# Kernel optimization log

Hardware: AMD Instinct MI355X
Metric: run time of the kernel (lower is better)

Reference implementation:

```python
import jax, jax.numpy as jnp
import numpy as np

NUM_HEADS = 8
NUM_GROUPS = 32
EPS = 1e-5


def setup_inputs() -> dict:
    key = jax.random.key(0)
    ks = jax.random.split(key, 6)
    C = 512
    scale = 1.0 / np.sqrt(C)
    return {
        "q": jax.random.normal(ks[0], (2, C, 64, 64), dtype=jnp.float32),
        "gn_w": jnp.ones((C,), jnp.float32),
        "gn_b": jnp.zeros((C,), jnp.float32),
        "wq": jax.random.normal(ks[1], (C, C), jnp.float32) * scale,
        "bq": jnp.zeros((C,), jnp.float32),
        "wk": jax.random.normal(ks[2], (C, C), jnp.float32) * scale,
        "bk": jnp.zeros((C,), jnp.float32),
        "wv": jax.random.normal(ks[3], (C, C), jnp.float32) * scale,
        "bv": jnp.zeros((C,), jnp.float32),
        "wo": jax.random.normal(ks[4], (C, C), jnp.float32) * scale,
        "bo": jnp.zeros((C,), jnp.float32),
    }


def _group_norm(x, w, b):
    # x: [B, C, H, W]
    B, C, H, W = x.shape
    xg = x.reshape(B, NUM_GROUPS, C // NUM_GROUPS, H, W)
    mean = xg.mean(axis=(2, 3, 4), keepdims=True)
    var = xg.var(axis=(2, 3, 4), keepdims=True)
    xn = ((xg - mean) * jax.lax.rsqrt(var + EPS)).reshape(B, C, H, W)
    return xn * w[None, :, None, None] + b[None, :, None, None]


def reference(q, gn_w, gn_b, wq, bq, wk, bk, wv, bv, wo, bo):
    B, C, H, W = q.shape
    hd = C // NUM_HEADS
    resid = q
    x = _group_norm(q, gn_w, gn_b)
    x = x.reshape(B, C, H * W).transpose(0, 2, 1)  # [B, N, C]
    # torch Linear: y = x @ W.T + b  (self-attention: k = v = x)
    qp = x @ wq.T + bq
    kp = x @ wk.T + bk
    vp = x @ wv.T + bv
    N = H * W
    def split(t):  # [B, N, C] -> [B, h, N, hd]
        return t.reshape(B, N, NUM_HEADS, hd).transpose(0, 2, 1, 3)
    qh, kh, vh = split(qp), split(kp), split(vp)
    scores = jnp.einsum('bhnc,bhmc->bhnm', qh, kh) / jnp.sqrt(jnp.float32(hd))
    attn = jax.nn.softmax(scores, axis=-1)
    out = jnp.einsum('bhnm,bhmc->bhnc', attn, vh)
    out = out.transpose(0, 2, 1, 3).reshape(B, N, C)
    out = out @ wo.T + bo
    out2d = out.transpose(0, 2, 1).reshape(B, C, H, W)
    return out2d + resid
```

## Files before the change

### kernel.cpp

```cpp
#include <hip/hip_runtime.h>
#include <hip/hip_bf16.h>
#include <cstdint>
#include <cstddef>

using bf16x8   = __attribute__((ext_vector_type(8))) short;
using f32x4    = __attribute__((ext_vector_type(4))) float;
using f32x16   = __attribute__((ext_vector_type(16))) float;
using ushort8  = __attribute__((ext_vector_type(8))) unsigned short;
using ushort4v = __attribute__((ext_vector_type(4))) unsigned short;
using float4v  = __attribute__((ext_vector_type(4))) float;
using float2v  = __attribute__((ext_vector_type(2))) float;

#define MFMA16(a,b,c) __builtin_amdgcn_mfma_f32_16x16x32_bf16((a),(b),(c),0,0,0)
#define MFMA32(a,b,c) __builtin_amdgcn_mfma_f32_32x32x16_bf16((a),(b),(c),0,0,0)

#define QSCALE 0.18033688011112042f

__device__ __forceinline__ unsigned short f2bf(float f){
    union { float f; unsigned u; } v; v.f = f;
    unsigned r = v.u + 0x7FFFu + ((v.u >> 16) & 1u);
    return (unsigned short)(r >> 16);
}

__device__ __forceinline__ int cvtpk(float lo, float hi){
    int r;
    asm volatile("v_cvt_pk_bf16_f32 %0, %1, %2" : "=v"(r) : "v"(lo), "v"(hi));
    return r;
}

#if __has_builtin(__builtin_amdgcn_permlane32_swap)
__device__ __forceinline__ void plswap(int &a, int &b){
    auto r = __builtin_amdgcn_permlane32_swap(a, b, false, false);
    a = r[0]; b = r[1];
}
#else
__device__ __forceinline__ void plswap(int &a, int &b){
    int ta = __shfl_xor(a, 32), tb = __shfl_xor(b, 32);
    bool hi = ((threadIdx.x & 63) >= 32);
    int na = hi ? tb : a;
    int nb = hi ? b  : ta;
    a = na; b = nb;
}
#endif

__device__ __forceinline__ void gload16(const unsigned short* g, unsigned short* l){
    __builtin_amdgcn_global_load_lds(
        (const __attribute__((address_space(1))) void*)g,
        (__attribute__((address_space(3))) void*)l,
        16, 0, 0);
}

__global__ __launch_bounds__(256) void gn_stats_wconv(const float* __restrict__ x,
                                                      float2v* __restrict__ parts,
                                                      const float* __restrict__ w0, const float* __restrict__ w1,
                                                      const float* __restrict__ w2, const float* __restrict__ w3,
                                                      unsigned short* wqk, unsigned short* wv, unsigned short* wo){
    int bid = blockIdx.x;
    if (bid < 512){
        const float4v* p4 = (const float4v*)(x + (size_t)bid * 8192);
        float s = 0.f, ss = 0.f;
        #pragma unroll
        for (int i = 0; i < 8; i++){
            float4v v = p4[i*256 + threadIdx.x];
            s  += v[0]+v[1]+v[2]+v[3];
            ss += v[0]*v[0]+v[1]*v[1]+v[2]*v[2]+v[3]*v[3];
        }
        __shared__ float ls[4], lss[4];
        int lane = threadIdx.x & 63, w = threadIdx.x >> 6;
        #pragma unroll
        for (int o = 32; o > 0; o >>= 1){ s += __shfl_down(s, o); ss += __shfl_down(ss, o); }
        if (lane == 0){ ls[w] = s; lss[w] = ss; }
        __syncthreads();
        if (threadIdx.x == 0){
            float2v p;
            p[0] = ls[0]+ls[1]+ls[2]+ls[3];
            p[1] = lss[0]+lss[1]+lss[2]+lss[3];
            parts[bid] = p;
        }
    } else {
        int i2 = bid - 512;
        int y = i2 >> 8, bx = i2 & 255;
        const float* src; unsigned short* dst; float sc = 1.0f;
        switch (y){
            case 0: src = w0; dst = wqk;          sc = QSCALE; break;
            case 1: src = w1; dst = wqk + 512*512; break;
            case 2: src = w2; dst = wv; break;
            default: src = w3; dst = wo; break;
        }
        int i = (bx*256 + threadIdx.x) * 4;
        float4v v = *(const float4v*)(src + i);
        ushort4v o;
        #pragma unroll
        for (int j = 0; j < 4; j++) o[j] = f2bf(v[j]*sc);
        *(ushort4v*)(dst + i) = o;
    }
}

__global__ __launch_bounds__(256) void gn_apply(const float* __restrict__ x,
                                                const float2v* __restrict__ parts,
                                                const float* __restrict__ gw,
                                                const float* __restrict__ gb,
                                                unsigned short* __restrict__ xn){
    int b = blockIdx.z, c0 = blockIdx.y * 64, n0 = blockIdx.x * 64;
    __shared__ unsigned short tile[64][68];
    __shared__ float gmean[4], grstd[4];
    if (threadIdx.x < 4){
        int g = b*32 + (c0 >> 4) + threadIdx.x;
        float s = 0.f, ss = 0.f;
        #pragma unroll
        for (int e = 0; e < 8; e++){
            float2v p = parts[g*8 + e];
            s += p[0]; ss += p[1];
        }
        float m = s * (1.f/65536.f);
        float var = ss * (1.f/65536.f) - m*m;
        gmean[threadIdx.x] = m;
        grstd[threadIdx.x] = rsqrtf(var + 1e-5f);
    }
    __syncthreads();
    for (int i = threadIdx.x; i < 64*16; i += 256){
        int row = i >> 4, f4 = i & 15;
        int c = c0 + row;
        int gl = row >> 4;
        float rs = grstd[gl];
        float wgt = gw[c] * rs;
        float bia = gb[c] - gmean[gl] * wgt;
        float4v v = *(const float4v*)(x + ((size_t)(b*512 + c))*4096 + n0 + f4*4);
        ushort4v o;
        #pragma unroll
        for (int j = 0; j < 4; j++) o[j] = f2bf(v[j]*wgt + bia);
        *(ushort4v*)&tile[row][f4*4] = o;
    }
    __syncthreads();
    for (int i = threadIdx.x; i < 64*8; i += 256){
        int nr = i >> 3, c8 = i & 7;
        ushort8 o;
        #pragma unroll
        for (int j = 0; j < 8; j++) o[j] = tile[c8*8 + j][nr];
        *(ushort8*)(xn + ((size_t)(b*4096 + n0 + nr))*512 + c0 + c8*8) = o;
    }
}

__global__ __launch_bounds__(256) void gemm_qkv(const unsigned short* __restrict__ xn,
                                                const unsigned short* __restrict__ wqk,
                                                const unsigned short* __restrict__ Wv,
                                                const float* __restrict__ bq,
                                                const float* __restrict__ bk,
                                                const float* __restrict__ bv,
                                                unsigned short* __restrict__ Q,
                                                unsigned short* __restrict__ K,
                                                unsigned short* __restrict__ Vt){
    __shared__ unsigned short Al[128*32];
    __shared__ unsigned short Bl[128*32];
    int bid = blockIdx.x;
    int t = threadIdx.x, lane = t & 63, w = t >> 6;
    int wr = w >> 1, wc = w & 1;
    int lr = lane >> 2, lc = lane & 3;

    if (bid < 512){
        int m0 = (bid & 63) * 128, n0 = (bid >> 6) * 128;
        f32x4 acc[4][4] = {};
        const unsigned short* Asrc = xn  + (size_t)(m0 + w*32 + lr)*512 + lc*8;
        const unsigned short* Bsrc = wqk + (size_t)(n0 + w*32 + lr)*512 + lc*8;
        unsigned short* Adst = &Al[(w*32)*32];
        unsigned short* Bdst = &Bl[(w*32)*32];

        for (int ks = 0; ks < 16; ks++){
            gload16(Asrc + ks*32,          Adst);
            gload16(Asrc + ks*32 + 16*512, Adst + 16*32);
            gload16(Bsrc + ks*32,          Bdst);
            gload16(Bsrc + ks*32 + 16*512, Bdst + 16*32);
            asm volatile("s_waitcnt vmcnt(0)" ::: "memory");
            __syncthreads();
            bf16x8 a[4], b[4];
            #pragma unroll
            for (int mi = 0; mi < 4; mi++) a[mi] = *(bf16x8*)&Al[(wr*64 + mi*16 + (lane&15))*32 + (lane>>4)*8];
            #pragma unroll
            for (int ni = 0; ni < 4; ni++) b[ni] = *(bf16x8*)&Bl[(wc*64 + ni*16 + (lane&15))*32 + (lane>>4)*8];
            #pragma unroll
            for (int mi = 0; mi < 4; mi++)
                #pragma unroll
                for (int ni = 0; ni < 4; ni++)
                    acc[mi][ni] = MFMA16(a[mi], b[ni], acc[mi][ni]);
            __syncthreads();
        }

        int cK = n0 >> 9;
        const float* bias = cK ? bk : bq;
        unsigned short* dst0 = cK ? K : Q;
        float bsc = cK ? 1.0f : QSCALE;
        #pragma unroll
        for (int mi = 0; mi < 4; mi++)
            #pragma unroll
            for (int ni = 0; ni < 4; ni++)
                #pragma unroll
                for (int r = 0; r < 4; r++){
                    int mrow = m0 + wr*64 + mi*16 + (lane>>4)*4 + r;
                    int col  = (n0 & 511) + wc*64 + ni*16 + (lane&15);
                    int b_ = mrow >> 12, n = mrow & 4095;
                    int h = col >> 6, d = col & 63;
                    float v = acc[mi][ni][r] + bias[col]*bsc;
                    dst0[(size_t)((b_*8+h)*4096 + n)*64 + d] = f2bf(v);
                }
    } else {
        int i2 = bid - 512;
        int m0 = (i2 >> 6) * 64, n0 = (i2 & 63) * 128;
        f32x4 acc[2][4] = {};
        const unsigned short* Asrc = Wv + (size_t)(m0 + w*16 + lr)*512 + lc*8;
        const unsigned short* Bsrc = xn + (size_t)(n0 + w*32 + lr)*512 + lc*8;
        unsigned short* Adst = &Al[(w*16)*32];
        unsigned short* Bdst = &Bl[(w*32)*32];

        for (int ks = 0; ks < 16; ks++){
            gload16(Asrc + ks*32,          Adst);
            gload16(Bsrc + ks*32,          Bdst);
            gload16(Bsrc + ks*32 + 16*512, Bdst + 16*32);
            asm volatile("s_waitcnt vmcnt(0)" ::: "memory");
            __syncthreads();
            bf16x8 a[2], b[4];
            #pragma unroll
            for (int mi = 0; mi < 2; mi++) a[mi] = *(bf16x8*)&Al[(wr*32 + mi*16 + (lane&15))*32 + (lane>>4)*8];
            #pragma unroll
            for (int ni = 0; ni < 4; ni++) b[ni] = *(bf16x8*)&Bl[(wc*64 + ni*16 + (lane&15))*32 + (lane>>4)*8];
            #pragma unroll
            for (int mi = 0; mi < 2; mi++)
                #pragma unroll
                for (int ni = 0; ni < 4; ni++)
                    acc[mi][ni] = MFMA16(a[mi], b[ni], acc[mi][ni]);
            __syncthreads();
        }
        #pragma unroll
        for (int mi = 0; mi < 2; mi++)
            #pragma unroll
            for (int ni = 0; ni < 4; ni++)
                #pragma unroll
                for (int r = 0; r < 4; r++){
                    int row  = m0 + wr*32 + mi*16 + (lane>>4)*4 + r;
                    int colm = n0 + wc*64 + ni*16 + (lane&15);
                    int b_ = colm >> 12, n = colm & 4095;
                    int h = row >> 6, d = row & 63;
                    float v = acc[mi][ni][r] + bv[row];
                    Vt[(size_t)((b_*8+h)*64 + d)*4096 + n] = f2bf(v);
                }
    }
}

__global__ __launch_bounds__(256) void gemm_o2(const unsigned short* __restrict__ Wo,
                                               const unsigned short* __restrict__ Om,
                                               const float* __restrict__ bo,
                                               const float* __restrict__ resid,
                                               float* __restrict__ outp){
    __shared__ unsigned short Al[64*32];
    __shared__ unsigned short Bl[128*32];
    int t = threadIdx.x, lane = t & 63, w = t >> 6;
    int wr = w >> 1, wc = w & 1;
    int m0 = blockIdx.y * 64, n0 = blockIdx.x * 128;
    int lr = lane >> 2, lc = lane & 3;
    f32x4 acc[2][4] = {};

    const unsigned short* Asrc = Wo + (size_t)(m0 + w*16 + lr)*512 + lc*8;
    const unsigned short* Bsrc = Om + (size_t)(n0 + w*32 + lr)*512 + lc*8;
    unsigned short* Adst = &Al[(w*16)*32];
    unsigned short* Bdst = &Bl[(w*32)*32];

    for (int ks = 0; ks < 16; ks++){
        gload16(Asrc + ks*32,          Adst);
        gload16(Bsrc + ks*32,          Bdst);
        gload16(Bsrc + ks*32 + 16*512, Bdst + 16*32);
        asm volatile("s_waitcnt vmcnt(0)" ::: "memory");
        __syncthreads();
        bf16x8 a[2], b[4];
        #pragma unroll
        for (int mi = 0; mi < 2; mi++) a[mi] = *(bf16x8*)&Al[(wr*32 + mi*16 + (lane&15))*32 + (lane>>4)*8];
        #pragma unroll
        for (int ni = 0; ni < 4; ni++) b[ni] = *(bf16x8*)&Bl[(wc*64 + ni*16 + (lane&15))*32 + (lane>>4)*8];
        #pragma unroll
        for (int mi = 0; mi < 2; mi++)
            #pragma unroll
            for (int ni = 0; ni < 4; ni++)
                acc[mi][ni] = MFMA16(a[mi], b[ni], acc[mi][ni]);
        __syncthreads();
    }
    #pragma unroll
    for (int mi = 0; mi < 2; mi++)
        #pragma unroll
        for (int ni = 0; ni < 4; ni++)
            #pragma unroll
            for (int r = 0; r < 4; r++){
                int row  = m0 + wr*32 + mi*16 + (lane>>4)*4 + r;
                int colm = n0 + wc*64 + ni*16 + (lane&15);
                int b_ = colm >> 12, n = colm & 4095;
                size_t oi = ((size_t)(b_*512 + row))*4096 + n;
                outp[oi] = acc[mi][ni][r] + bo[row] + resid[oi];
            }
}

__global__ __launch_bounds__(128, 2) void attn9(const unsigned short* __restrict__ Q,
                                                const unsigned short* __restrict__ K,
                                                const unsigned short* __restrict__ Vt,
                                                unsigned short* __restrict__ O){
    int bid = blockIdx.x;
    int idx = bid >> 3;
    int bh = ((bid & 7) << 1) | (idx >> 6);
    int qt = idx & 63;
    int t = threadIdx.x, lane = t & 63, w = t >> 6;
    int ln = lane & 31, hi = lane >> 5;
    int q0 = qt * 64;

    __shared__ unsigned short Kl[2][64*64];
    __shared__ unsigned short Vl[2][2][64*32];

    const unsigned short* Qb = Q  + (size_t)bh * 4096 * 64;
    const unsigned short* Kb = K  + (size_t)bh * 4096 * 64;
    const unsigned short* Vb = Vt + (size_t)bh * 64 * 4096;

    bf16x8 bqa[4], bqb[4];
    #pragma unroll
    for (int dsub = 0; dsub < 4; dsub++){
        bqa[dsub] = *(const bf16x8*)(Qb + (size_t)(q0 + ln)*64      + dsub*16 + hi*8);
        bqb[dsub] = *(const bf16x8*)(Qb + (size_t)(q0 + 32 + ln)*64 + dsub*16 + hi*8);
    }

    int srow = lane >> 3;
    int sswz = (lane & 7) ^ srow;
    int vdl = lane >> 2;
    int vsl = (lane & 3) ^ ((vdl >> 1) & 3);

    auto stage = [&](int kt){
        int kv0 = kt * 64;
        unsigned short* kdst = &Kl[kt & 1][0];
        #pragma unroll
        for (int i = 0; i < 4; i++){
            int r0 = w*32 + i*8;
            gload16(Kb + (size_t)(kv0 + r0 + srow)*64 + sswz*8, kdst + r0*64);
        }
        unsigned short* vdst = &Vl[kt & 1][w][0];
        #pragma unroll
        for (int i = 0; i < 4; i++)
            gload16(Vb + (size_t)(i*16 + vdl)*4096 + kv0 + w*32 + vsl*8, vdst + i*512);
    };

    stage(0);
    stage(1);

    f32x16 o0a, o1a, o0b, o1b, z;
    #pragma unroll
    for (int r = 0; r < 16; r++){ o0a[r]=0.f; o1a[r]=0.f; o0b[r]=0.f; o1b[r]=0.f; z[r]=0.f; }
    float lsA = 0.f, lsB = 0.f;

    const char* KbA = (const char*)&Kl[0][0] + (w*32 + ln)*128;
    int swzr = (ln & 7) << 4;
    const char* VbW = (const char*)&Vl[0][w][0];
    int vrswz = (ln >> 1) & 3;

    for (int kt = 0; kt < 64; kt++){
        if (kt < 63) asm volatile("s_waitcnt vmcnt(8)" ::: "memory");
        else         asm volatile("s_waitcnt vmcnt(0)" ::: "memory");
        __builtin_amdgcn_sched_barrier(0);

        int kboff = (kt & 1) * (64*64*2);
        int vboff = (kt & 1) * (2*64*32*2);

        f32x16 sA, sB;
        {
            int cb = (hi*16) ^ swzr;
            bf16x8 ak = *(const bf16x8*)(KbA + kboff + cb);
            sA = MFMA32(ak, bqa[0], z);
            sB = MFMA32(ak, bqb[0], z);
        }
        __builtin_amdgcn_s_setprio(1);
        #pragma unroll
        for (int dsub = 1; dsub < 4; dsub++){
            int cb = (dsub*32 + hi*16) ^ swzr;
            bf16x8 ak = *(const bf16x8*)(KbA + kboff + cb);
            sA = MFMA32(ak, bqa[dsub], sA);
            sB = MFMA32(ak, bqb[dsub], sB);
        }
        __builtin_amdgcn_s_setprio(0);

        #pragma unroll
        for (int r = 0; r < 16; r++){ sA[r] = __builtin_amdgcn_exp2f(sA[r]); lsA += sA[r]; }
        #pragma unroll
        for (int r = 0; r < 16; r++){ sB[r] = __builtin_amdgcn_exp2f(sB[r]); lsB += sB[r]; }

        __builtin_amdgcn_s_setprio(1);
        #pragma unroll
        for (int hsel = 0; hsel < 2; hsel++){
            int obp = hsel * 8;
            int a0 = cvtpk(sA[obp+0], sA[obp+1]);
            int a1 = cvtpk(sA[obp+2], sA[obp+3]);
            int c0 = cvtpk(sA[obp+4], sA[obp+5]);
            int c1 = cvtpk(sA[obp+6], sA[obp+7]);
            plswap(a0, c0);
            plswap(a1, c1);
            union { int i[4]; bf16x8 v; } fuA;
            fuA.i[0] = a0; fuA.i[1] = a1; fuA.i[2] = c0; fuA.i[3] = c1;

            int d0 = cvtpk(sB[obp+0], sB[obp+1]);
            int d1 = cvtpk(sB[obp+2], sB[obp+3]);
            int e0 = cvtpk(sB[obp+4], sB[obp+5]);
            int e1 = cvtpk(sB[obp+6], sB[obp+7]);
            plswap(d0, e0);
            plswap(d1, e1);
            union { int i[4]; bf16x8 v; } fuB;
            fuB.i[0] = d0; fuB.i[1] = d1; fuB.i[2] = e0; fuB.i[3] = e1;

            int p0 = (((hsel*2 + hi) ^ vrswz) << 4);
            bf16x8 av0 = *(const bf16x8*)(VbW + vboff + ln*64 + p0);
            bf16x8 av1 = *(const bf16x8*)(VbW + vboff + (32 + ln)*64 + p0);
            o0a = MFMA32(av0, fuA.v, o0a);
            o1a = MFMA32(av1, fuA.v, o1a);
            o0b = MFMA32(av0, fuB.v, o0b);
            o1b = MFMA32(av1, fuB.v, o1b);
        }
        __builtin_amdgcn_s_setprio(0);

        __builtin_amdgcn_sched_barrier(0);
        if (kt < 62) stage(kt + 2);
        __builtin_amdgcn_sched_barrier(0);
    }

    lsA += __shfl_xor(lsA, 32);
    lsB += __shfl_xor(lsB, 32);
    __syncthreads();
    float* m1 = (float*)&Kl[0][0];
    float* m2 = (float*)&Vl[0][0][0];
    if (w == 1){
        #pragma unroll
        for (int r = 0; r < 16; r++){
            m1[r*64 + lane]        = o0a[r];
            m1[1024 + r*64 + lane] = o1a[r];
            m2[r*64 + lane]        = o0b[r];
            m2[1024 + r*64 + lane] = o1b[r];
        }
        if (hi == 0){ m2[2048 + ln] = lsA; m2[2048 + 32 + ln] = lsB; }
    }
    __syncthreads();
    if (w == 0){
        #pragma unroll
        for (int r = 0; r < 16; r++){
            o0a[r] += m1[r*64 + lane];
            o1a[r] += m1[1024 + r*64 + lane];
            o0b[r] += m2[r*64 + lane];
            o1b[r] += m2[1024 + r*64 + lane];
        }
        float rA = 1.0f / (lsA + m2[2048 + ln]);
        float rB = 1.0f / (lsB + m2[2048 + 32 + ln]);
        int b = bh >> 3, h = bh & 7;
        unsigned short* dstA = O + (size_t)(b*4096 + q0 + ln)*512      + h*64;
        unsigned short* dstB = O + (size_t)(b*4096 + q0 + 32 + ln)*512 + h*64;
        #pragma unroll
        for (int m = 0; m < 2; m++){
            const f32x16& ovA = m ? o1a : o0a;
            const f32x16& ovB = m ? o1b : o0b;
            #pragma unroll
            for (int g = 0; g < 4; g++){
                int d = m*32 + g*8 + hi*4;
                ushort4v pkA, pkB;
                #pragma unroll
                for (int j = 0; j < 4; j++){
                    pkA[j] = f2bf(ovA[g*4 + j] * rA);
                    pkB[j] = f2bf(ovB[g*4 + j] * rB);
                }
                *(ushort4v*)(dstA + d) = pkA;
                *(ushort4v*)(dstB + d) = pkB;
            }
        }
    }
}

extern "C" void kernel_launch(void* const* d_in, const int* in_sizes, int n_in,
                              void* d_out, int out_size, void* d_ws, size_t ws_size,
                              hipStream_t stream) {
    const float* q    = (const float*)d_in[0];
    const float* gn_w = (const float*)d_in[1];
    const float* gn_b = (const float*)d_in[2];
    const float* wq   = (const float*)d_in[3];
    const float* bq   = (const float*)d_in[4];
    const float* wk   = (const float*)d_in[5];
    const float* bk   = (const float*)d_in[6];
    const float* wv   = (const float*)d_in[7];
    const float* bv   = (const float*)d_in[8];
    const float* wo   = (const float*)d_in[9];
    const float* bo   = (const float*)d_in[10];
    float* outp = (float*)d_out;

    char* ws = (char*)d_ws;
    float2v* parts = (float2v*)ws;
    unsigned short* xn  = (unsigned short*)(ws + 8192);
    const size_t TOK = (size_t)8192 * 512;
    unsigned short* wqkb = xn + TOK;
    unsigned short* wvb  = wqkb + 1024*512;
    unsigned short* wob  = wvb + 512*512;
    unsigned short* Qb   = wob + 512*512;
    unsigned short* Kb   = Qb + TOK;
    unsigned short* Vt   = Kb + TOK;
    unsigned short* Ob   = Vt + TOK;

    gn_stats_wconv<<<1536, 256, 0, stream>>>(q, parts, wq, wk, wv, wo, wqkb, wvb, wob);
    gn_apply<<<dim3(64, 8, 2), 256, 0, stream>>>(q, parts, gn_w, gn_b, xn);
    gemm_qkv<<<1024, 256, 0, stream>>>(xn, wqkb, wvb, bq, bk, bv, Qb, Kb, Vt);
    attn9<<<1024, 128, 0, stream>>>(Qb, Kb, Vt, Ob);
    gemm_o2<<<dim3(64, 8), 256, 0, stream>>>(wob, Ob, bo, q, outp);
}
```

Baseline: 134.2 us.

## Single-buffer V tile in attention to cut LDS and raise occupancy

Turns the V tile from a double buffer into a single buffer. V for step kt+1 is staged right after step kt finishes using V, while K keeps its two-ahead prefetch. This halves the V LDS footprint and raises the launch_bounds minimum blocks per CU from 2 to 3, so more waves can hide latency. In exchange, V loads get only one iteration of lead time, and the wait count is cut to match. The epilogue reduction scratch is remapped to fit the smaller V buffer.

```diff
diff --git a/kernel.cpp b/kernel.cpp
--- a/kernel.cpp
+++ b/kernel.cpp
@@ -295,10 +295,10 @@
             }
 }
 
-__global__ __launch_bounds__(128, 2) void attn9(const unsigned short* __restrict__ Q,
-                                                const unsigned short* __restrict__ K,
-                                                const unsigned short* __restrict__ Vt,
-                                                unsigned short* __restrict__ O){
+__global__ __launch_bounds__(128, 3) void attn10(const unsigned short* __restrict__ Q,
+                                                 const unsigned short* __restrict__ K,
+                                                 const unsigned short* __restrict__ Vt,
+                                                 unsigned short* __restrict__ O){
     int bid = blockIdx.x;
     int idx = bid >> 3;
     int bh = ((bid & 7) << 1) | (idx >> 6);
@@ -308,7 +308,7 @@
     int q0 = qt * 64;
 
     __shared__ unsigned short Kl[2][64*64];
-    __shared__ unsigned short Vl[2][2][64*32];
+    __shared__ unsigned short Vl[2][64*32];
 
     const unsigned short* Qb = Q  + (size_t)bh * 4096 * 64;
     const unsigned short* Kb = K  + (size_t)bh * 4096 * 64;
@@ -326,7 +326,7 @@
     int vdl = lane >> 2;
     int vsl = (lane & 3) ^ ((vdl >> 1) & 3);
 
-    auto stage = [&](int kt){
+    auto stageK = [&](int kt){
         int kv0 = kt * 64;
         unsigned short* kdst = &Kl[kt & 1][0];
         #pragma unroll
@@ -334,14 +334,18 @@
             int r0 = w*32 + i*8;
             gload16(Kb + (size_t)(kv0 + r0 + srow)*64 + sswz*8, kdst + r0*64);
         }
-        unsigned short* vdst = &Vl[kt & 1][w][0];
+    };
+    auto stageV = [&](int kt){
+        int kv0 = kt * 64;
+        unsigned short* vdst = &Vl[w][0];
         #pragma unroll
         for (int i = 0; i < 4; i++)
             gload16(Vb + (size_t)(i*16 + vdl)*4096 + kv0 + w*32 + vsl*8, vdst + i*512);
     };
 
-    stage(0);
-    stage(1);
+    stageK(0);
+    stageV(0);
+    stageK(1);
 
     f32x16 o0a, o1a, o0b, o1b, z;
     #pragma unroll
@@ -350,16 +354,15 @@
 
     const char* KbA = (const char*)&Kl[0][0] + (w*32 + ln)*128;
     int swzr = (ln & 7) << 4;
-    const char* VbW = (const char*)&Vl[0][w][0];
+    const char* VbW = (const char*)&Vl[w][0];
     int vrswz = (ln >> 1) & 3;
 
     for (int kt = 0; kt < 64; kt++){
-        if (kt < 63) asm volatile("s_waitcnt vmcnt(8)" ::: "memory");
+        if (kt < 63) asm volatile("s_waitcnt vmcnt(4)" ::: "memory");
         else         asm volatile("s_waitcnt vmcnt(0)" ::: "memory");
         __builtin_amdgcn_sched_barrier(0);
 
         int kboff = (kt & 1) * (64*64*2);
-        int vboff = (kt & 1) * (2*64*32*2);
 
         f32x16 sA, sB;
         {
@@ -406,8 +409,8 @@
             fuB.i[0] = d0; fuB.i[1] = d1; fuB.i[2] = e0; fuB.i[3] = e1;
 
             int p0 = (((hsel*2 + hi) ^ vrswz) << 4);
-            bf16x8 av0 = *(const bf16x8*)(VbW + vboff + ln*64 + p0);
-            bf16x8 av1 = *(const bf16x8*)(VbW + vboff + (32 + ln)*64 + p0);
+            bf16x8 av0 = *(const bf16x8*)(VbW + ln*64 + p0);
+            bf16x8 av1 = *(const bf16x8*)(VbW + (32 + ln)*64 + p0);
             o0a = MFMA32(av0, fuA.v, o0a);
             o1a = MFMA32(av1, fuA.v, o1a);
             o0b = MFMA32(av0, fuB.v, o0b);
@@ -416,7 +419,8 @@
         __builtin_amdgcn_s_setprio(0);
 
         __builtin_amdgcn_sched_barrier(0);
-        if (kt < 62) stage(kt + 2);
+        if (kt < 63) stageV(kt + 1);
+        if (kt < 62) stageK(kt + 2);
         __builtin_amdgcn_sched_barrier(0);
     }
 
@@ -424,16 +428,16 @@
     lsB += __shfl_xor(lsB, 32);
     __syncthreads();
     float* m1 = (float*)&Kl[0][0];
-    float* m2 = (float*)&Vl[0][0][0];
+    float* m2 = (float*)&Vl[0][0];
     if (w == 1){
         #pragma unroll
         for (int r = 0; r < 16; r++){
             m1[r*64 + lane]        = o0a[r];
             m1[1024 + r*64 + lane] = o1a[r];
-            m2[r*64 + lane]        = o0b[r];
-            m2[1024 + r*64 + lane] = o1b[r];
-        }
-        if (hi == 0){ m2[2048 + ln] = lsA; m2[2048 + 32 + ln] = lsB; }
+            m1[2048 + r*64 + lane] = o0b[r];
+            m1[3072 + r*64 + lane] = o1b[r];
+        }
+        if (hi == 0){ m2[ln] = lsA; m2[32 + ln] = lsB; }
     }
     __syncthreads();
     if (w == 0){
@@ -441,11 +445,11 @@
         for (int r = 0; r < 16; r++){
             o0a[r] += m1[r*64 + lane];
             o1a[r] += m1[1024 + r*64 + lane];
-            o0b[r] += m2[r*64 + lane];
-            o1b[r] += m2[1024 + r*64 + lane];
-        }
-        float rA = 1.0f / (lsA + m2[2048 + ln]);
-        float rB = 1.0f / (lsB + m2[2048 + 32 + ln]);
+            o0b[r] += m1[2048 + r*64 + lane];
+            o1b[r] += m1[3072 + r*64 + lane];
+        }
+        float rA = 1.0f / (lsA + m2[ln]);
+        float rB = 1.0f / (lsB + m2[32 + ln]);
         int b = bh >> 3, h = bh & 7;
         unsigned short* dstA = O + (size_t)(b*4096 + q0 + ln)*512      + h*64;
         unsigned short* dstB = O + (size_t)(b*4096 + q0 + 32 + ln)*512 + h*64;
@@ -500,6 +504,6 @@
     gn_stats_wconv<<<1536, 256, 0, stream>>>(q, parts, wq, wk, wv, wo, wqkb, wvb, wob);
     gn_apply<<<dim3(64, 8, 2), 256, 0, stream>>>(q, parts, gn_w, gn_b, xn);
     gemm_qkv<<<1024, 256, 0, stream>>>(xn, wqkb, wvb, bq, bk, bv, Qb, Kb, Vt);
-    attn9<<<1024, 128, 0, stream>>>(Qb, Kb, Vt, Ob);
+    attn10<<<1024, 128, 0, stream>>>(Qb, Kb, Vt, Ob);
     gemm_o2<<<dim3(64, 8), 256, 0, stream>>>(wob, Ob, bo, q, outp);
 }
```

New measurement: 172.0 us. 28.1% more time.

## Software-pipeline attention loop so next QK^T overlaps current softmax and PV

Applied to the files above, without the earlier changes.

Restructures the attention main loop into a two-tile software pipeline. The QK^T MFMAs for tile t+1 are issued alongside the exp/convert/PV work for tile t, and K and V staging are split so each is fetched on its own schedule. The aim is to keep the matrix units busy while the exp and pack work runs. It adds a second live score accumulator pair, which raises register pressure, and the new waitcnt accounting has to stay correct across the split K/V loads. The setprio hints are dropped.

```diff
diff --git a/kernel.cpp b/kernel.cpp
--- a/kernel.cpp
+++ b/kernel.cpp
@@ -295,10 +295,10 @@
             }
 }
 
-__global__ __launch_bounds__(128, 2) void attn9(const unsigned short* __restrict__ Q,
-                                                const unsigned short* __restrict__ K,
-                                                const unsigned short* __restrict__ Vt,
-                                                unsigned short* __restrict__ O){
+__global__ __launch_bounds__(128, 2) void attn11(const unsigned short* __restrict__ Q,
+                                                 const unsigned short* __restrict__ K,
+                                                 const unsigned short* __restrict__ Vt,
+                                                 unsigned short* __restrict__ O){
     int bid = blockIdx.x;
     int idx = bid >> 3;
     int bh = ((bid & 7) << 1) | (idx >> 6);
@@ -326,7 +326,7 @@
     int vdl = lane >> 2;
     int vsl = (lane & 3) ^ ((vdl >> 1) & 3);
 
-    auto stage = [&](int kt){
+    auto stageK = [&](int kt){
         int kv0 = kt * 64;
         unsigned short* kdst = &Kl[kt & 1][0];
         #pragma unroll
@@ -334,16 +334,16 @@
             int r0 = w*32 + i*8;
             gload16(Kb + (size_t)(kv0 + r0 + srow)*64 + sswz*8, kdst + r0*64);
         }
+    };
+    auto stageV = [&](int kt){
+        int kv0 = kt * 64;
         unsigned short* vdst = &Vl[kt & 1][w][0];
         #pragma unroll
         for (int i = 0; i < 4; i++)
             gload16(Vb + (size_t)(i*16 + vdl)*4096 + kv0 + w*32 + vsl*8, vdst + i*512);
     };
 
-    stage(0);
-    stage(1);
-
-    f32x16 o0a, o1a, o0b, o1b, z;
+    f32x16 o0a, o1a, o0b, o1b, z, sEA, sEB, sOA, sOB;
     #pragma unroll
     for (int r = 0; r < 16; r++){ o0a[r]=0.f; o1a[r]=0.f; o0b[r]=0.f; o1b[r]=0.f; z[r]=0.f; }
     float lsA = 0.f, lsB = 0.f;
@@ -352,73 +352,95 @@
     int swzr = (ln & 7) << 4;
     const char* VbW = (const char*)&Vl[0][w][0];
     int vrswz = (ln >> 1) & 3;
-
-    for (int kt = 0; kt < 64; kt++){
-        if (kt < 63) asm volatile("s_waitcnt vmcnt(8)" ::: "memory");
-        else         asm volatile("s_waitcnt vmcnt(0)" ::: "memory");
+    const int KBUFSZ = 64*64*2;
+    const int VBUFSZ = 2*64*32*2;
+
+#define QKSTEP(SA,SB, KBOFF) { \
+    { int cb = (hi*16) ^ swzr; \
+      bf16x8 ak = *(const bf16x8*)(KbA + (KBOFF) + cb); \
+      SA = MFMA32(ak, bqa[0], z); \
+      SB = MFMA32(ak, bqb[0], z); } \
+    _Pragma("unroll") \
+    for (int dsub = 1; dsub < 4; dsub++){ \
+        int cb = (dsub*32 + hi*16) ^ swzr; \
+        bf16x8 ak = *(const bf16x8*)(KbA + (KBOFF) + cb); \
+        SA = MFMA32(ak, bqa[dsub], SA); \
+        SB = MFMA32(ak, bqb[dsub], SB); \
+    } }
+
+#define FINISH(SA,SB, VBOFF) { \
+    _Pragma("unroll") \
+    for (int r = 0; r < 16; r++){ SA[r] = __builtin_amdgcn_exp2f(SA[r]); lsA += SA[r]; } \
+    _Pragma("unroll") \
+    for (int r = 0; r < 16; r++){ SB[r] = __builtin_amdgcn_exp2f(SB[r]); lsB += SB[r]; } \
+    _Pragma("unroll") \
+    for (int hsel = 0; hsel < 2; hsel++){ \
+        int obp = hsel * 8; \
+        int a0 = cvtpk(SA[obp+0], SA[obp+1]); \
+        int a1 = cvtpk(SA[obp+2], SA[obp+3]); \
+        int c0 = cvtpk(SA[obp+4], SA[obp+5]); \
+        int c1 = cvtpk(SA[obp+6], SA[obp+7]); \
+        plswap(a0, c0); plswap(a1, c1); \
+        union { int i[4]; bf16x8 v; } fuA; \
+        fuA.i[0] = a0; fuA.i[1] = a1; fuA.i[2] = c0; fuA.i[3] = c1; \
+        int d0 = cvtpk(SB[obp+0], SB[obp+1]); \
+        int d1 = cvtpk(SB[obp+2], SB[obp+3]); \
+        int e0 = cvtpk(SB[obp+4], SB[obp+5]); \
+        int e1 = cvtpk(SB[obp+6], SB[obp+7]); \
+        plswap(d0, e0); plswap(d1, e1); \
+        union { int i[4]; bf16x8 v; } fuB; \
+        fuB.i[0] = d0; fuB.i[1] = d1; fuB.i[2] = e0; fuB.i[3] = e1; \
+        int p0 = (((hsel*2 + hi) ^ vrswz) << 4); \
+        bf16x8 av0 = *(const bf16x8*)(VbW + (VBOFF) + ln*64 + p0); \
+        bf16x8 av1 = *(const bf16x8*)(VbW + (VBOFF) + (32 + ln)*64 + p0); \
+        o0a = MFMA32(av0, fuA.v, o0a); \
+        o1a = MFMA32(av1, fuA.v, o1a); \
+        o0b = MFMA32(av0, fuB.v, o0b); \
+        o1b = MFMA32(av1, fuB.v, o1b); \
+    } }
+
+    stageK(0);
+    stageV(0);
+    stageK(1);
+
+    asm volatile("s_waitcnt vmcnt(8)" ::: "memory");
+    __builtin_amdgcn_sched_barrier(0);
+    QKSTEP(sEA, sEB, 0)
+    __builtin_amdgcn_sched_barrier(0);
+    stageV(1);
+    stageK(2);
+    __builtin_amdgcn_sched_barrier(0);
+
+    for (int tt = 0; tt < 31; tt++){
+        int t1 = 2*tt + 1;
+        asm volatile("s_waitcnt vmcnt(8)" ::: "memory");
         __builtin_amdgcn_sched_barrier(0);
-
-        int kboff = (kt & 1) * (64*64*2);
-        int vboff = (kt & 1) * (2*64*32*2);
-
-        f32x16 sA, sB;
-        {
-            int cb = (hi*16) ^ swzr;
-            bf16x8 ak = *(const bf16x8*)(KbA + kboff + cb);
-            sA = MFMA32(ak, bqa[0], z);
-            sB = MFMA32(ak, bqb[0], z);
-        }
-        __builtin_amdgcn_s_setprio(1);
-        #pragma unroll
-        for (int dsub = 1; dsub < 4; dsub++){
-            int cb = (dsub*32 + hi*16) ^ swzr;
-            bf16x8 ak = *(const bf16x8*)(KbA + kboff + cb);
-            sA = MFMA32(ak, bqa[dsub], sA);
-            sB = MFMA32(ak, bqb[dsub], sB);
-        }
-        __builtin_amdgcn_s_setprio(0);
-
-        #pragma unroll
-        for (int r = 0; r < 16; r++){ sA[r] = __builtin_amdgcn_exp2f(sA[r]); lsA += sA[r]; }
-        #pragma unroll
-        for (int r = 0; r < 16; r++){ sB[r] = __builtin_amdgcn_exp2f(sB[r]); lsB += sB[r]; }
-
-        __builtin_amdgcn_s_setprio(1);
-        #pragma unroll
-        for (int hsel = 0; hsel < 2; hsel++){
-            int obp = hsel * 8;
-            int a0 = cvtpk(sA[obp+0], sA[obp+1]);
-            int a1 = cvtpk(sA[obp+2], sA[obp+3]);
-            int c0 = cvtpk(sA[obp+4], sA[obp+5]);
-            int c1 = cvtpk(sA[obp+6], sA[obp+7]);
-            plswap(a0, c0);
-            plswap(a1, c1);
-            union { int i[4]; bf16x8 v; } fuA;
-            fuA.i[0] = a0; fuA.i[1] = a1; fuA.i[2] = c0; fuA.i[3] = c1;
-
-            int d0 = cvtpk(sB[obp+0], sB[obp+1]);
-            int d1 = cvtpk(sB[obp+2], sB[obp+3]);
-            int e0 = cvtpk(sB[obp+4], sB[obp+5]);
-            int e1 = cvtpk(sB[obp+6], sB[obp+7]);
-            plswap(d0, e0);
-            plswap(d1, e1);
-            union { int i[4]; bf16x8 v; } fuB;
-            fuB.i[0] = d0; fuB.i[1] = d1; fuB.i[2] = e0; fuB.i[3] = e1;
-
-            int p0 = (((hsel*2 + hi) ^ vrswz) << 4);
-            bf16x8 av0 = *(const bf16x8*)(VbW + vboff + ln*64 + p0);
-            bf16x8 av1 = *(const bf16x8*)(VbW + vboff + (32 + ln)*64 + p0);
-            o0a = MFMA32(av0, fuA.v, o0a);
-            o1a = MFMA32(av1, fuA.v, o1a);
-            o0b = MFMA32(av0, fuB.v, o0b);
-            o1b = MFMA32(av1, fuB.v, o1b);
-        }
-        __builtin_amdgcn_s_setprio(0);
-
+        QKSTEP(sOA, sOB, KBUFSZ)
+        FINISH(sEA, sEB, 0)
         __builtin_amdgcn_sched_barrier(0);
-        if (kt < 62) stage(kt + 2);
+        stageV(t1 + 1);
+        stageK(t1 + 2);
         __builtin_amdgcn_sched_barrier(0);
-    }
+        asm volatile("s_waitcnt vmcnt(8)" ::: "memory");
+        __builtin_amdgcn_sched_barrier(0);
+        QKSTEP(sEA, sEB, 0)
+        FINISH(sOA, sOB, VBUFSZ)
+        __builtin_amdgcn_sched_barrier(0);
+        stageV(t1 + 2);
+        if (tt < 30) stageK(t1 + 3);
+        __builtin_amdgcn_sched_barrier(0);
+    }
+
+    asm volatile("s_waitcnt vmcnt(4)" ::: "memory");
+    __builtin_amdgcn_sched_barrier(0);
+    QKSTEP(sOA, sOB, KBUFSZ)
+    FINISH(sEA, sEB, 0)
+    asm volatile("s_waitcnt vmcnt(0)" ::: "memory");
+    __builtin_amdgcn_sched_barrier(0);
+    FINISH(sOA, sOB, VBUFSZ)
+
+#undef QKSTEP
+#undef FINISH
 
     lsA += __shfl_xor(lsA, 32);
     lsB += __shfl_xor(lsB, 32);
@@ -500,6 +522,6 @@
     gn_stats_wconv<<<1536, 256, 0, stream>>>(q, parts, wq, wk, wv, wo, wqkb, wvb, wob);
     gn_apply<<<dim3(64, 8, 2), 256, 0, stream>>>(q, parts, gn_w, gn_b, xn);
     gemm_qkv<<<1024, 256, 0, stream>>>(xn, wqkb, wvb, bq, bk, bv, Qb, Kb, Vt);
-    attn9<<<1024, 128, 0, stream>>>(Qb, Kb, Vt, Ob);
+    attn11<<<1024, 128, 0, stream>>>(Qb, Kb, Vt, Ob);
     gemm_o2<<<dim3(64, 8), 256, 0, stream>>>(wob, Ob, bo, q, outp);
 }
```

Result: no change. 133.6 us (-0.5%).
